# Kernel tuning notes

Hardware: AMD Instinct MI355X
Metric: run time of the kernel (lower is better)

## Reference

```python
import jax, jax.numpy as jnp
import numpy as np

K = 9
STRIDE = 1
UNFOLDINGS = 12
N_SIGMA = 1
SIGMA_MIN, SIGMA_MAX = 0.0, 50.0


def soft_threshold(x, lmbda):
    return jnp.sign(x) * jnp.maximum(jnp.abs(x) - lmbda, 0.0)


def lookup_arr(value):
    # arr = [sigma_min + d*i for i in range(n_sigma+1)], d=(max-min)/n_sigma
    d = (SIGMA_MAX - SIGMA_MIN) / N_SIGMA
    arr = [SIGMA_MIN + d * i for i in range(N_SIGMA + 1)]
    for i, x in enumerate(arr):
        if value <= x:
            return max(i - 1, 0)
    return len(arr) - 2


def im2col(I, k, s):
    # torch F.unfold ordering: channel-major, then kh, kw -> [B, C*k*k, Ho, Wo]
    B, C, H, W = I.shape
    Ho = (H - k) // s + 1
    Wo = (W - k) // s + 1
    cols = jnp.stack(
        [I[:, :, i:i + (Ho - 1) * s + 1:s, j:j + (Wo - 1) * s + 1:s]
         for i in range(k) for j in range(k)], axis=2)  # [B, C, k*k, Ho, Wo]
    return cols.reshape(B, C * k * k, Ho, Wo)


def col2im_avg(cols, H, W, k, s):
    # F.fold with averaging by overlap counts
    B, Ckk, Ho, Wo = cols.shape
    C = Ckk // (k * k)
    x = cols.reshape(B, C, k, k, Ho, Wo)
    out = jnp.zeros((B, C, H, W), cols.dtype)
    cnt = jnp.zeros((1, 1, H, W), cols.dtype)
    one = jnp.ones((1, 1, Ho, Wo), cols.dtype)
    for i in range(k):
        for j in range(k):
            sl_h = slice(i, i + (Ho - 1) * s + 1, s)
            sl_w = slice(j, j + (Wo - 1) * s + 1, s)
            out = out.at[:, :, sl_h, sl_w].add(x[:, :, i, j])
            cnt = cnt.at[:, :, sl_h, sl_w].add(one)
    return out / cnt


def setup_inputs() -> dict:
    key = jax.random.key(0)
    k1, k2 = jax.random.split(key)
    Ckk = K * K * 3  # 243
    F = 256
    I = jax.random.normal(k1, (4, 3, 128, 128), dtype=jnp.float32)
    # Dictionary init normalized by sqrt of top singular value ~ spectral norm
    D = jax.random.normal(k2, (Ckk, F), dtype=jnp.float32)
    s_max = jnp.linalg.norm(D.T @ D, ord=2)
    D = D / jnp.sqrt(s_max)
    A = D.T                      # [F, Ckk]
    Dw = jnp.array(D)            # [Ckk, F]
    Ww = jnp.array(D)            # [Ckk, F]
    lmbdas = jnp.full((UNFOLDINGS, F), 0.01, dtype=jnp.float32)
    return {"I": I, "A": A, "Dw": Dw, "Ww": Ww, "lmbdas": lmbdas, "sigma_hat": 25}


def reference(I, A, Dw, Ww, lmbdas, sigma_hat):
    noise_set = lookup_arr(sigma_hat)  # python int, trace-time constant
    B, C, H, W = I.shape
    I_col = im2col(I, K, STRIDE)                     # [B, Ckk, Ho, Wo]
    mean_patch = I_col.mean(axis=1, keepdims=True)   # centered patches
    I_c = I_col - mean_patch
    lin = jnp.einsum('fc,bchw->bfhw', A, I_c)
    lm = lmbdas[noise_set * UNFOLDINGS][None, :, None, None]
    gamma = soft_threshold(lin, lm)
    for kk in range(UNFOLDINGS - 1):
        x_k = jnp.einsum('cf,bfhw->bchw', Dw, gamma)
        r_k = jnp.einsum('fc,bchw->bfhw', A, x_k - I_c)
        lm = lmbdas[noise_set * UNFOLDINGS + kk + 1][None, :, None, None]
        gamma = soft_threshold(gamma - r_k, lm)
    out_all = jnp.einsum('cf,bfhw->bchw', Ww, gamma) + mean_patch
    return col2im_avg(out_all, H, W, K, STRIDE)
```

## Files before the change

### kernel.cpp

```cpp
#include <hip/hip_runtime.h>
#include <stdint.h>

typedef __attribute__((ext_vector_type(8))) short bf16x8;
typedef __attribute__((ext_vector_type(4))) float f32x4;

__device__ __forceinline__ unsigned short f2bf(float f) {
  union { float f; unsigned u; } v; v.f = f;
  unsigned u = v.u;
  u += 0x7fffu + ((u >> 16) & 1u);
  return (unsigned short)(u >> 16);
}
__device__ __forceinline__ float bfpk_lo(unsigned pk) {
  union { unsigned u; float f; } v; v.u = pk << 16; return v.f;
}
__device__ __forceinline__ float bfpk_hi(unsigned pk) {
  union { unsigned u; float f; } v; v.u = pk & 0xffff0000u; return v.f;
}

__device__ __forceinline__ int swz_idx(int k, int n) {
  return ((((k >> 5) * 16 + (n >> 4)) * 64) + (((k >> 3) & 3) * 16 + (n & 15))) * 8 + (k & 7);
}

#define ST_STRIDE 272

__device__ __attribute__((aligned(16))) unsigned short g_Acswz[65536];
__device__ __attribute__((aligned(16))) unsigned short g_Gswz[65536];
__device__ __attribute__((aligned(16))) unsigned short g_W3swz[65536];

__global__ void prep_all(const float* __restrict__ A, const float* __restrict__ Dw,
                         const float* __restrict__ Ww, float* __restrict__ out) {
  __shared__ float red[256];
  const int b = blockIdx.x;
  const int tid = threadIdx.x;
  out[b * 256 + tid] = 0.f;

  if (b < 256) {
    float s = 0.f;
    for (int c = tid; c < 243; c += 256) s += A[b * 243 + c];
    red[tid] = s;
    __syncthreads();
    for (int off = 128; off; off >>= 1) {
      if (tid < off) red[tid] += red[tid + off];
      __syncthreads();
    }
    float rm = red[0] * (1.f / 243.f);
    int k = tid;
    float v = 0.f;
    if (k < 243) {
      int rw = k / 9, j = k - rw * 9;
      int i = rw / 3, c = rw - i * 3;
      int corig = c * 81 + i * 9 + j;
      v = A[b * 243 + corig] - rm;
    }
    g_Acswz[swz_idx(k, b)] = f2bf(v);
  } else if (b < 512) {
    int f = b - 256, fp = tid;
    float s = 0.f;
    for (int c = 0; c < 243; ++c) s += A[f * 243 + c] * Dw[c * 256 + fp];
    g_Gswz[swz_idx(fp, f)] = f2bf(((f == fp) ? 1.f : 0.f) - s);
  } else {
    int cc = b - 512, f = tid;
    float v = 0.f;
    if (cc < 243) {
      int rw = cc / 9, j = cc - rw * 9;
      int i = rw / 3, c = rw - i * 3;
      int corig = c * 81 + i * 9 + j;
      v = Ww[corig * 256 + f];
    }
    g_W3swz[swz_idx(f, cc)] = f2bf(v);
  }
}

template <int CMODE>
__device__ __forceinline__ void run_gemm(const unsigned short* __restrict__ Bsrc,
                                         const unsigned short* stg, int w, int lane,
                                         int m, int q, f32x4 (&acc)[4][4],
                                         const unsigned (&linpk)[4][4][2]) {
  bf16x8 bcur[4];
#pragma unroll
  for (int un = 0; un < 4; ++un)
    bcur[un] = *(const bf16x8*)(Bsrc + (((4 * w + un) * 64 + lane) << 3));
#pragma unroll
  for (int s = 0; s < 8; ++s) {
    bf16x8 bnext[4];
    if (s < 7) {
#pragma unroll
      for (int un = 0; un < 4; ++un)
        bnext[un] = *(const bf16x8*)(Bsrc + ((((s + 1) * 16 + 4 * w + un) * 64 + lane) << 3));
    }
#pragma unroll
    for (int t = 0; t < 4; ++t) {
      bf16x8 afr = *(const bf16x8*)(stg + (t * 16 + m) * ST_STRIDE + s * 32 + q * 8);
#pragma unroll
      for (int un = 0; un < 4; ++un) {
        f32x4 cin;
        if (s == 0) {
          if (CMODE == 1) {
            cin[0] = bfpk_lo(linpk[t][un][0]);
            cin[1] = bfpk_hi(linpk[t][un][0]);
            cin[2] = bfpk_lo(linpk[t][un][1]);
            cin[3] = bfpk_hi(linpk[t][un][1]);
          } else {
            cin = (f32x4){0.f, 0.f, 0.f, 0.f};
          }
        } else {
          cin = acc[t][un];
        }
        acc[t][un] = __builtin_amdgcn_mfma_f32_16x16x32_bf16(afr, bcur[un], cin, 0, 0, 0);
      }
    }
    if (s < 7) {
#pragma unroll
      for (int un = 0; un < 4; ++un) bcur[un] = bnext[un];
    }
  }
}

__global__ __launch_bounds__(256, 2) void lista_fused(
    const float* __restrict__ I, const float* __restrict__ lmb, float* __restrict__ out) {
  __shared__ __attribute__((aligned(16))) unsigned short stage[2][64 * ST_STRIDE];
  __shared__ float img[3][16][16];
  __shared__ float meanv[64];
  __shared__ float outacc[768];

  const int tid = threadIdx.x;
  const int lane = tid & 63;
  const int w = tid >> 6;
  const int m = lane & 15;
  const int q = lane >> 4;

  const int blk = blockIdx.x;
  const int b = blk / 225;
  const int t2 = blk - b * 225;
  const int ty = t2 / 15;
  const int tx = t2 - ty * 15;
  const int py0 = ty * 8, px0 = tx * 8;

  const float* Ib = I + b * (3 * 128 * 128);
  for (int r = tid; r < 768; r += 256) {
    int c = r >> 8;
    int yx = r & 255;
    int y = yx >> 4, x = yx & 15;
    img[c][y][x] = Ib[c * 16384 + (py0 + y) * 128 + (px0 + x)];
    outacc[r] = 0.f;
  }
  if (tid < 64) meanv[tid] = 0.f;
  __syncthreads();

  {
    const int pos = tid & 63;
    const int part = tid >> 6;
    const int y = pos >> 3, x = pos & 7;
    int j = part, c = 0, i = 0;
    float s = 0.f;
    unsigned short* srow = &stage[0][pos * ST_STRIDE];
    for (int kk = 0; kk < 64; ++kk) {
      int k = part + 4 * kk;
      float v = 0.f;
      if (k < 243) { v = img[c][y + i][x + j]; s += v; }
      srow[k] = f2bf(v);
      j += 4;
      if (j >= 9) { j -= 9; if (++c == 3) { c = 0; ++i; } }
    }
    atomicAdd(&meanv[pos], s * (1.f / 243.f));
  }
  __syncthreads();

  f32x4 acc[4][4];
  unsigned linpk[4][4][2];

  run_gemm<0>(g_Acswz, stage[0], w, lane, m, q, acc, linpk);

#pragma unroll
  for (int un = 0; un < 4; ++un) {
    int f = 64 * w + un * 16 + m;
    float lam = lmb[f];
#pragma unroll
    for (int t = 0; t < 4; ++t) {
      linpk[t][un][0] = (unsigned)f2bf(acc[t][un][0]) | ((unsigned)f2bf(acc[t][un][1]) << 16);
      linpk[t][un][1] = (unsigned)f2bf(acc[t][un][2]) | ((unsigned)f2bf(acc[t][un][3]) << 16);
#pragma unroll
      for (int r = 0; r < 4; ++r) {
        float x0 = acc[t][un][r];
        float g = x0 - fminf(fmaxf(x0, -lam), lam);
        stage[1][(t * 16 + q * 4 + r) * ST_STRIDE + f] = f2bf(g);
      }
    }
  }
  __syncthreads();

  for (int kk = 0; kk < 11; ++kk) {
    const int rb = (kk & 1) ^ 1;
    run_gemm<1>(g_Gswz, stage[rb], w, lane, m, q, acc, linpk);
#pragma unroll
    for (int un = 0; un < 4; ++un) {
      int f = 64 * w + un * 16 + m;
      float lam = lmb[(kk + 1) * 256 + f];
#pragma unroll
      for (int t = 0; t < 4; ++t)
#pragma unroll
        for (int r = 0; r < 4; ++r) {
          float x0 = acc[t][un][r];
          float g = x0 - fminf(fmaxf(x0, -lam), lam);
          stage[rb ^ 1][(t * 16 + q * 4 + r) * ST_STRIDE + f] = f2bf(g);
        }
    }
    __syncthreads();
  }

  run_gemm<0>(g_W3swz, stage[0], w, lane, m, q, acc, linpk);

#pragma unroll
  for (int un = 0; un < 4; ++un) {
    int cc = 64 * w + un * 16 + m;
    if (cc < 243) {
      int rw = cc / 9, jj = cc - rw * 9;
      int i = rw / 3, c = rw - i * 3;
#pragma unroll
      for (int t = 0; t < 4; ++t)
#pragma unroll
        for (int r = 0; r < 4; ++r) {
          int pos = t * 16 + q * 4 + r;
          int y = (pos >> 3) + i, x = (pos & 7) + jj;
          float val = acc[t][un][r] + meanv[pos];
          atomicAdd(&outacc[c * 256 + y * 16 + x], val);
        }
    }
  }
  __syncthreads();

  float* Ob = out + b * (3 * 128 * 128);
  for (int r = tid; r < 768; r += 256) {
    int c = r >> 8;
    int yx = r & 255;
    int y = yx >> 4, x = yx & 15;
    atomicAdd(&Ob[c * 16384 + (py0 + y) * 128 + (px0 + x)], outacc[r]);
  }
}

__global__ void div_counts(float* __restrict__ out, int n) {
  int idx = blockIdx.x * 256 + threadIdx.x;
  if (idx >= n) return;
  int x = idx & 127, y = (idx >> 7) & 127;
  int loy = y - 8; if (loy < 0) loy = 0;
  int hiy = y; if (hiy > 119) hiy = 119;
  int lox = x - 8; if (lox < 0) lox = 0;
  int hix = x; if (hix > 119) hix = 119;
  float cnt = (float)((hiy - loy + 1) * (hix - lox + 1));
  out[idx] = out[idx] / cnt;
}

extern "C" void kernel_launch(void* const* d_in, const int* in_sizes, int n_in,
                              void* d_out, int out_size, void* d_ws, size_t ws_size,
                              hipStream_t stream) {
  const float* I = (const float*)d_in[0];
  const float* A = (const float*)d_in[1];
  const float* Dw = (const float*)d_in[2];
  const float* Ww = (const float*)d_in[3];
  const float* lmb = (const float*)d_in[4];
  float* out = (float*)d_out;
  (void)d_ws; (void)ws_size;

  prep_all<<<768, 256, 0, stream>>>(A, Dw, Ww, out);
  lista_fused<<<900, 256, 0, stream>>>(I, lmb, out);
  div_counts<<<768, 256, 0, stream>>>(out, out_size);
}
```

Before: 279.7 us.

## Single-buffer LDS staging, alias image/output buffers, raise occupancy to 4 blocks

Replaces the double-buffered gamma staging area with a single buffer and adds a barrier after each GEMM so the buffer can be overwritten safely. The image tile buffer is reused as the output accumulator. Together these cut LDS use per block so four blocks can fit per CU, and launch bounds are raised to match. Bf16 conversion now uses the packed v_cvt_pk_bf16_f32 instruction, and the soft-threshold outputs are written in pairs. The cost is one extra block-wide barrier per iteration, plus tighter register limits that could cause spills.

```diff
diff --git a/kernel.cpp b/kernel.cpp
--- a/kernel.cpp
+++ b/kernel.cpp
@@ -15,6 +15,14 @@
 }
 __device__ __forceinline__ float bfpk_hi(unsigned pk) {
   union { unsigned u; float f; } v; v.u = pk & 0xffff0000u; return v.f;
+}
+__device__ __forceinline__ unsigned cvt_pk_bf16(float lo, float hi) {
+  unsigned r;
+  asm("v_cvt_pk_bf16_f32 %0, %1, %2" : "=v"(r) : "v"(lo), "v"(hi));
+  return r;
+}
+__device__ __forceinline__ float soft_th(float x, float lam) {
+  return x - fminf(fmaxf(x, -lam), lam);
 }
 
 __device__ __forceinline__ int swz_idx(int k, int n) {
@@ -116,12 +124,11 @@
   }
 }
 
-__global__ __launch_bounds__(256, 2) void lista_fused(
+__global__ __launch_bounds__(256, 4) void lista_fused(
     const float* __restrict__ I, const float* __restrict__ lmb, float* __restrict__ out) {
-  __shared__ __attribute__((aligned(16))) unsigned short stage[2][64 * ST_STRIDE];
-  __shared__ float img[3][16][16];
+  __shared__ __attribute__((aligned(16))) unsigned short stage[64 * ST_STRIDE];
+  __shared__ __attribute__((aligned(16))) float ibuf[768];
   __shared__ float meanv[64];
-  __shared__ float outacc[768];
 
   const int tid = threadIdx.x;
   const int lane = tid & 63;
@@ -141,8 +148,7 @@
     int c = r >> 8;
     int yx = r & 255;
     int y = yx >> 4, x = yx & 15;
-    img[c][y][x] = Ib[c * 16384 + (py0 + y) * 128 + (px0 + x)];
-    outacc[r] = 0.f;
+    ibuf[r] = Ib[c * 16384 + (py0 + y) * 128 + (px0 + x)];
   }
   if (tid < 64) meanv[tid] = 0.f;
   __syncthreads();
@@ -153,11 +159,11 @@
     const int y = pos >> 3, x = pos & 7;
     int j = part, c = 0, i = 0;
     float s = 0.f;
-    unsigned short* srow = &stage[0][pos * ST_STRIDE];
+    unsigned short* srow = &stage[pos * ST_STRIDE];
     for (int kk = 0; kk < 64; ++kk) {
       int k = part + 4 * kk;
       float v = 0.f;
-      if (k < 243) { v = img[c][y + i][x + j]; s += v; }
+      if (k < 243) { v = ibuf[c * 256 + (y + i) * 16 + (x + j)]; s += v; }
       srow[k] = f2bf(v);
       j += 4;
       if (j >= 9) { j -= 9; if (++c == 3) { c = 0; ++i; } }
@@ -166,49 +172,55 @@
   }
   __syncthreads();
 
+  for (int r = tid; r < 768; r += 256) ibuf[r] = 0.f;
+
   f32x4 acc[4][4];
   unsigned linpk[4][4][2];
 
-  run_gemm<0>(g_Acswz, stage[0], w, lane, m, q, acc, linpk);
+  run_gemm<0>(g_Acswz, stage, w, lane, m, q, acc, linpk);
+  __syncthreads();
 
 #pragma unroll
   for (int un = 0; un < 4; ++un) {
     int f = 64 * w + un * 16 + m;
     float lam = lmb[f];
+    unsigned short* sp = &stage[(q * 4) * ST_STRIDE + f];
 #pragma unroll
     for (int t = 0; t < 4; ++t) {
-      linpk[t][un][0] = (unsigned)f2bf(acc[t][un][0]) | ((unsigned)f2bf(acc[t][un][1]) << 16);
-      linpk[t][un][1] = (unsigned)f2bf(acc[t][un][2]) | ((unsigned)f2bf(acc[t][un][3]) << 16);
-#pragma unroll
-      for (int r = 0; r < 4; ++r) {
-        float x0 = acc[t][un][r];
-        float g = x0 - fminf(fmaxf(x0, -lam), lam);
-        stage[1][(t * 16 + q * 4 + r) * ST_STRIDE + f] = f2bf(g);
-      }
+      linpk[t][un][0] = cvt_pk_bf16(acc[t][un][0], acc[t][un][1]);
+      linpk[t][un][1] = cvt_pk_bf16(acc[t][un][2], acc[t][un][3]);
+      unsigned p01 = cvt_pk_bf16(soft_th(acc[t][un][0], lam), soft_th(acc[t][un][1], lam));
+      unsigned p23 = cvt_pk_bf16(soft_th(acc[t][un][2], lam), soft_th(acc[t][un][3], lam));
+      sp[(t * 16 + 0) * ST_STRIDE] = (unsigned short)p01;
+      sp[(t * 16 + 1) * ST_STRIDE] = (unsigned short)(p01 >> 16);
+      sp[(t * 16 + 2) * ST_STRIDE] = (unsigned short)p23;
+      sp[(t * 16 + 3) * ST_STRIDE] = (unsigned short)(p23 >> 16);
     }
   }
   __syncthreads();
 
   for (int kk = 0; kk < 11; ++kk) {
-    const int rb = (kk & 1) ^ 1;
-    run_gemm<1>(g_Gswz, stage[rb], w, lane, m, q, acc, linpk);
+    run_gemm<1>(g_Gswz, stage, w, lane, m, q, acc, linpk);
+    __syncthreads();
 #pragma unroll
     for (int un = 0; un < 4; ++un) {
       int f = 64 * w + un * 16 + m;
       float lam = lmb[(kk + 1) * 256 + f];
-#pragma unroll
-      for (int t = 0; t < 4; ++t)
-#pragma unroll
-        for (int r = 0; r < 4; ++r) {
-          float x0 = acc[t][un][r];
-          float g = x0 - fminf(fmaxf(x0, -lam), lam);
-          stage[rb ^ 1][(t * 16 + q * 4 + r) * ST_STRIDE + f] = f2bf(g);
-        }
+      unsigned short* sp = &stage[(q * 4) * ST_STRIDE + f];
+#pragma unroll
+      for (int t = 0; t < 4; ++t) {
+        unsigned p01 = cvt_pk_bf16(soft_th(acc[t][un][0], lam), soft_th(acc[t][un][1], lam));
+        unsigned p23 = cvt_pk_bf16(soft_th(acc[t][un][2], lam), soft_th(acc[t][un][3], lam));
+        sp[(t * 16 + 0) * ST_STRIDE] = (unsigned short)p01;
+        sp[(t * 16 + 1) * ST_STRIDE] = (unsigned short)(p01 >> 16);
+        sp[(t * 16 + 2) * ST_STRIDE] = (unsigned short)p23;
+        sp[(t * 16 + 3) * ST_STRIDE] = (unsigned short)(p23 >> 16);
+      }
     }
     __syncthreads();
   }
 
-  run_gemm<0>(g_W3swz, stage[0], w, lane, m, q, acc, linpk);
+  run_gemm<0>(g_W3swz, stage, w, lane, m, q, acc, linpk);
 
 #pragma unroll
   for (int un = 0; un < 4; ++un) {
@@ -223,7 +235,7 @@
           int pos = t * 16 + q * 4 + r;
           int y = (pos >> 3) + i, x = (pos & 7) + jj;
           float val = acc[t][un][r] + meanv[pos];
-          atomicAdd(&outacc[c * 256 + y * 16 + x], val);
+          atomicAdd(&ibuf[c * 256 + y * 16 + x], val);
         }
     }
   }
@@ -234,7 +246,7 @@
     int c = r >> 8;
     int yx = r & 255;
     int y = yx >> 4, x = yx & 15;
-    atomicAdd(&Ob[c * 16384 + (py0 + y) * 128 + (px0 + x)], outacc[r]);
+    atomicAdd(&Ob[c * 16384 + (py0 + y) * 128 + (px0 + x)], ibuf[r]);
   }
 }
 
```

Measured after the change: 408.4 us. 46.0% more time.
